# Kernel tuning notes

Measured on AMD Instinct MI355X. Metric: run time of the kernel, lower is better.

Reference implementation:

```python
import jax, jax.numpy as jnp
import numpy as np

NUM_EXPERTS = 64
TOP_K = 8
NORM_TOPK_PROB = True


def setup_inputs() -> dict:
    key = jax.random.key(0)
    k1, k2 = jax.random.split(key)
    hidden_states = jax.random.normal(k1, (8192, 4096), dtype=jnp.float32)
    gate_w = jax.random.normal(k2, (NUM_EXPERTS, 4096), dtype=jnp.float32) * (1.0 / np.sqrt(4096))
    return {"hidden_states": hidden_states, "gate_w": gate_w}


def reference(hidden_states, gate_w):
    # router_logits: (T, E) = hidden @ gate_w.T
    router_logits = jnp.einsum('th,eh->te', hidden_states, gate_w)
    # softmax in float32 (matches F.softmax(..., dtype=torch.float32))
    router_probs = jax.nn.softmax(router_logits.astype(jnp.float32), axis=-1)
    # top-k selection (descending, like torch.topk)
    expert_weights, expert_indices = jax.lax.top_k(router_probs, TOP_K)
    if NORM_TOPK_PROB:
        expert_weights = expert_weights / jnp.sum(expert_weights, axis=-1, keepdims=True)
    expert_weights = expert_weights.astype(hidden_states.dtype)
    # load-balancing loss: N_e * sum_i f_i * p_i
    num_tokens = router_probs.shape[0]
    one_hot = jax.nn.one_hot(expert_indices, NUM_EXPERTS, dtype=jnp.float32)  # (T, K, E)
    tokens_per_expert = one_hot.sum(axis=(0, 1))                              # (E,)
    f = tokens_per_expert / (num_tokens * TOP_K)
    p = router_probs.mean(axis=0)
    aux_loss = NUM_EXPERTS * jnp.sum(f * p)
    return (expert_weights, expert_indices, aux_loss)
```

## Files before the change

### kernel.cpp

```cpp
#include <hip/hip_runtime.h>
#include <math.h>

#define HDIM 4096
#define NEXP 64
#define NTOK 8192
#define KSPLIT 8
#define KSLICE (HDIM / KSPLIT)
#define BM 128
#define CHUNK 32
#define NCHUNK (KSLICE / CHUNK)
#define ASTRIDE 40
#define SLICEOFF 1024
#define TPW 2

typedef short short8 __attribute__((ext_vector_type(8)));
typedef float f32x4 __attribute__((ext_vector_type(4)));

__device__ __forceinline__ void split2x3(float x0, float x1, int& h, int& md, int& lo) {
  unsigned u0 = __float_as_uint(x0), u1 = __float_as_uint(x1);
  unsigned h0 = u0 & 0xFFFF0000u, h1 = u1 & 0xFFFF0000u;
  float r0 = x0 - __uint_as_float(h0);
  float r1 = x1 - __uint_as_float(h1);
  unsigned m0 = __float_as_uint(r0) & 0xFFFF0000u;
  unsigned m1 = __float_as_uint(r1) & 0xFFFF0000u;
  float s0 = r0 - __uint_as_float(m0);
  float s1 = r1 - __uint_as_float(m1);
  h  = (int)((h0 >> 16) | h1);
  md = (int)((m0 >> 16) | m1);
  lo = (int)((__float_as_uint(s0) >> 16) | (__float_as_uint(s1) & 0xFFFF0000u));
}

__global__ __launch_bounds__(256, 3) void gemm_k(const float* __restrict__ A,
                                                 const float* __restrict__ W,
                                                 float* __restrict__ Lp,
                                                 int atomic_mode) {
  __shared__ __align__(16) short Ah[BM * ASTRIDE], Amid[BM * ASTRIDE], Alo[BM * ASTRIDE];
  __shared__ __align__(16) short Bh[NEXP * ASTRIDE], Bmid[NEXP * ASTRIDE], Blo[NEXP * ASTRIDE];
  const int tid = threadIdx.x;
  const int m_base = blockIdx.x * BM;
  const int k_base = blockIdx.y * KSLICE;
  float* Lout = Lp + (atomic_mode ? (size_t)0 : (size_t)blockIdx.y * NTOK * NEXP);

  const int srow = tid >> 2;
  const int skg = tid & 3;
  const float* gA0 = A + (size_t)(m_base + srow) * HDIM + k_base + skg * 8;
  const float* gA1 = gA0 + (size_t)64 * HDIM;
  const float* gB = W + (size_t)srow * HDIM + k_base + skg * 8;

  const int lane = tid & 63;
  const int wave = tid >> 6;
  const int l15 = lane & 15;
  const int quad = lane >> 4;
  const int wm = wave * 32;

  f32x4 acc[2][4];
#pragma unroll
  for (int mt = 0; mt < 2; ++mt)
#pragma unroll
    for (int nt = 0; nt < 4; ++nt) acc[mt][nt] = (f32x4){0.f, 0.f, 0.f, 0.f};

  float4 pa0[2], pa1[2], pb[2];
  auto gload = [&](int i) {
    const float* p = gA0 + i * CHUNK;
    pa0[0] = *(const float4*)(p);
    pa0[1] = *(const float4*)(p + 4);
    p = gA1 + i * CHUNK;
    pa1[0] = *(const float4*)(p);
    pa1[1] = *(const float4*)(p + 4);
    p = gB + i * CHUNK;
    pb[0] = *(const float4*)(p);
    pb[1] = *(const float4*)(p + 4);
  };
  auto convert_store = [&]() {
    const float fa0[8] = {pa0[0].x, pa0[0].y, pa0[0].z, pa0[0].w,
                          pa0[1].x, pa0[1].y, pa0[1].z, pa0[1].w};
    const float fa1[8] = {pa1[0].x, pa1[0].y, pa1[0].z, pa1[0].w,
                          pa1[1].x, pa1[1].y, pa1[1].z, pa1[1].w};
    const float fb[8] = {pb[0].x, pb[0].y, pb[0].z, pb[0].w,
                         pb[1].x, pb[1].y, pb[1].z, pb[1].w};
    int h[4], md[4], lo[4];
    int off = srow * ASTRIDE + skg * 8;
#pragma unroll
    for (int j = 0; j < 4; ++j) split2x3(fa0[2 * j], fa0[2 * j + 1], h[j], md[j], lo[j]);
    *(int4*)&Ah[off] = make_int4(h[0], h[1], h[2], h[3]);
    *(int4*)&Amid[off] = make_int4(md[0], md[1], md[2], md[3]);
    *(int4*)&Alo[off] = make_int4(lo[0], lo[1], lo[2], lo[3]);
#pragma unroll
    for (int j = 0; j < 4; ++j) split2x3(fa1[2 * j], fa1[2 * j + 1], h[j], md[j], lo[j]);
    int off1 = (srow + 64) * ASTRIDE + skg * 8;
    *(int4*)&Ah[off1] = make_int4(h[0], h[1], h[2], h[3]);
    *(int4*)&Amid[off1] = make_int4(md[0], md[1], md[2], md[3]);
    *(int4*)&Alo[off1] = make_int4(lo[0], lo[1], lo[2], lo[3]);
#pragma unroll
    for (int j = 0; j < 4; ++j) split2x3(fb[2 * j], fb[2 * j + 1], h[j], md[j], lo[j]);
    *(int4*)&Bh[off] = make_int4(h[0], h[1], h[2], h[3]);
    *(int4*)&Bmid[off] = make_int4(md[0], md[1], md[2], md[3]);
    *(int4*)&Blo[off] = make_int4(lo[0], lo[1], lo[2], lo[3]);
  };

  gload(0);
  convert_store();
  __syncthreads();

  for (int i = 0; i < NCHUNK; ++i) {
    if (i + 1 < NCHUNK) gload(i + 1);
    short8 fa[2][3];
#pragma unroll
    for (int mt = 0; mt < 2; ++mt) {
      const int r = (wm + mt * 16 + l15) * ASTRIDE + quad * 8;
      fa[mt][0] = *(const short8*)&Ah[r];
      fa[mt][1] = *(const short8*)&Amid[r];
      fa[mt][2] = *(const short8*)&Alo[r];
    }
#pragma unroll
    for (int nt = 0; nt < 4; ++nt) {
      const int r = (nt * 16 + l15) * ASTRIDE + quad * 8;
      const short8 bh = *(const short8*)&Bh[r];
      const short8 bm = *(const short8*)&Bmid[r];
      const short8 bl = *(const short8*)&Blo[r];
#pragma unroll
      for (int mt = 0; mt < 2; ++mt) {
        f32x4 c = acc[mt][nt];
        c = __builtin_amdgcn_mfma_f32_16x16x32_bf16(fa[mt][0], bh, c, 0, 0, 0);
        c = __builtin_amdgcn_mfma_f32_16x16x32_bf16(fa[mt][0], bm, c, 0, 0, 0);
        c = __builtin_amdgcn_mfma_f32_16x16x32_bf16(fa[mt][1], bh, c, 0, 0, 0);
        c = __builtin_amdgcn_mfma_f32_16x16x32_bf16(fa[mt][0], bl, c, 0, 0, 0);
        c = __builtin_amdgcn_mfma_f32_16x16x32_bf16(fa[mt][2], bh, c, 0, 0, 0);
        c = __builtin_amdgcn_mfma_f32_16x16x32_bf16(fa[mt][1], bm, c, 0, 0, 0);
        acc[mt][nt] = c;
      }
    }
    __syncthreads();
    if (i + 1 < NCHUNK) convert_store();
    __syncthreads();
  }

#pragma unroll
  for (int mt = 0; mt < 2; ++mt)
#pragma unroll
    for (int nt = 0; nt < 4; ++nt)
#pragma unroll
      for (int r = 0; r < 4; ++r) {
        const int m = m_base + wm + mt * 16 + quad * 4 + r;
        const int n = nt * 16 + l15;
        if (atomic_mode) atomicAdd(&Lout[(size_t)m * NEXP + n], acc[mt][nt][r]);
        else Lout[(size_t)m * NEXP + n] = acc[mt][nt][r];
      }
}

__global__ __launch_bounds__(256) void topk_k(const float* __restrict__ Lp, int nsl,
                                              float* __restrict__ out,
                                              float* __restrict__ auxbuf) {
  __shared__ float sl[4][64];
  __shared__ float s_aux[128];
  const int tid = threadIdx.x;
  const int wave = tid >> 6, lane = tid & 63;
  if (tid < 128) s_aux[tid] = 0.f;
  __syncthreads();

  for (int it = 0; it < TPW; ++it) {
    const int t = (blockIdx.x * 4 + wave) * TPW + it;
    float x = 0.f;
    for (int s = 0; s < nsl; ++s)
      x += Lp[(size_t)s * (NTOK * NEXP) + (size_t)t * NEXP + lane];
    sl[wave][lane] = x;

    float mx = x;
#pragma unroll
    for (int off = 32; off >= 1; off >>= 1)
      mx = fmaxf(mx, __shfl_xor(mx, off, 64));
    const float e = __expf(x - mx);
    float ssum = e;
#pragma unroll
    for (int off = 32; off >= 1; off >>= 1) ssum += __shfl_xor(ssum, off, 64);
    const float prob = e / ssum;

    __syncthreads();

    int cnt = 0;
#pragma unroll
    for (int c = 0; c < 4; ++c) {
      const float4 v0 = *(const float4*)&sl[wave][c * 16 + 0];
      const float4 v1 = *(const float4*)&sl[wave][c * 16 + 4];
      const float4 v2 = *(const float4*)&sl[wave][c * 16 + 8];
      const float4 v3 = *(const float4*)&sl[wave][c * 16 + 12];
      const float xv[16] = {v0.x, v0.y, v0.z, v0.w, v1.x, v1.y, v1.z, v1.w,
                            v2.x, v2.y, v2.z, v2.w, v3.x, v3.y, v3.z, v3.w};
#pragma unroll
      for (int j = 0; j < 16; ++j) {
        const int jj = c * 16 + j;
        cnt += (xv[j] > x) || (xv[j] == x && jj < lane);
      }
    }

    float tp = (cnt < 8) ? prob : 0.f;
    float tsum = tp;
#pragma unroll
    for (int off = 32; off >= 1; off >>= 1) tsum += __shfl_xor(tsum, off, 64);

    const int dst = cnt << 2;
    const float pv = __uint_as_float(
        (unsigned)__builtin_amdgcn_ds_permute(dst, (int)__float_as_uint(prob)));
    const int pi = __builtin_amdgcn_ds_permute(dst, lane);
    if (lane < 8) {
      out[(size_t)t * 8 + lane] = pv / tsum;
      out[(size_t)NTOK * 8 + (size_t)t * 8 + lane] = (float)pi;
    }
    atomicAdd(&s_aux[lane], prob);
    if (cnt < 8) atomicAdd(&s_aux[64 + lane], 1.f);
  }
  __syncthreads();
  if (tid < 128) atomicAdd(&auxbuf[(blockIdx.x & 7) * 128 + tid], s_aux[tid]);
}

__global__ void aux_k(const float* __restrict__ auxbuf, float* __restrict__ out) {
  const int e = threadIdx.x;
  float p = 0.f, f = 0.f;
#pragma unroll
  for (int c = 0; c < 8; ++c) {
    p += auxbuf[c * 128 + e];
    f += auxbuf[c * 128 + 64 + e];
  }
  p *= (1.f / (float)NTOK);
  f *= (1.f / ((float)NTOK * 8.f));
  float v = f * p;
#pragma unroll
  for (int off = 32; off >= 1; off >>= 1) v += __shfl_xor(v, off, 64);
  if (e == 0) out[2 * NTOK * 8] = 64.f * v;
}

extern "C" void kernel_launch(void* const* d_in, const int* in_sizes, int n_in,
                              void* d_out, int out_size, void* d_ws, size_t ws_size,
                              hipStream_t stream) {
  const float* hidden = (const float*)d_in[0];
  const float* gate = (const float*)d_in[1];
  float* out = (float*)d_out;
  float* ws = (float*)d_ws;
  float* auxbuf = ws;
  float* slices = ws + SLICEOFF;

  const size_t need = (size_t)SLICEOFF * 4 + (size_t)KSPLIT * NTOK * NEXP * 4;
  const int atomic_mode = (ws_size < need) ? 1 : 0;
  const int nsl = atomic_mode ? 1 : KSPLIT;

  if (atomic_mode)
    hipMemsetAsync(d_ws, 0, (size_t)SLICEOFF * 4 + (size_t)NTOK * NEXP * 4, stream);
  else
    hipMemsetAsync(d_ws, 0, (size_t)SLICEOFF * 4, stream);

  gemm_k<<<dim3(64, KSPLIT), 256, 0, stream>>>(hidden, gate, slices, atomic_mode);
  topk_k<<<NTOK / (4 * TPW), 256, 0, stream>>>(slices, nsl, out, auxbuf);
  aux_k<<<1, 64, 0, stream>>>(auxbuf, out);
}
```

Before: 217.6 us.

## Pre-split gate weights into bf16x3 layout and split A on the fly

Adds a small pre-kernel that splits gate_w into high, mid and low bf16 parts laid out per 32-wide K chunk. The GEMM then reads B fragments straight from global memory. A is staged in LDS as raw fp32 in a double buffer and split into bf16 parts per wave just before the MFMAs, which drops one barrier per iteration. The top-k slice reduction is also unrolled for the 8-slice case. This removes the per-block redundant conversion of B and some LDS traffic, at the cost of an extra launch, global B loads in the inner loop, and repeated A splitting across waves.

```diff
diff --git a/kernel.cpp b/kernel.cpp
--- a/kernel.cpp
+++ b/kernel.cpp
@@ -9,8 +9,12 @@
 #define BM 128
 #define CHUNK 32
 #define NCHUNK (KSLICE / CHUNK)
-#define ASTRIDE 40
-#define SLICEOFF 1024
+#define AROW 36
+#define PSTRIDE 2048
+#define CSTRIDE 6144
+#define AUXF 1024
+#define BSF 393216
+#define SLICEOFF (AUXF + BSF)
 #define TPW 2
 
 typedef short short8 __attribute__((ext_vector_type(8)));
@@ -30,22 +34,45 @@
   lo = (int)((__float_as_uint(s0) >> 16) | (__float_as_uint(s1) & 0xFFFF0000u));
 }
 
+__device__ __forceinline__ short8 pack_s8(int a, int b, int c, int d) {
+  union { int i[4]; short8 s; } u;
+  u.i[0] = a; u.i[1] = b; u.i[2] = c; u.i[3] = d;
+  return u.s;
+}
+
+__global__ void bsplit_k(const float* __restrict__ W, short* __restrict__ Bs) {
+  const int e = blockIdx.x;
+  const int tid = threadIdx.x;
+#pragma unroll
+  for (int it = 0; it < 2; ++it) {
+    const int k0 = tid * 16 + it * 8;
+    const float4 v0 = *(const float4*)&W[(size_t)e * HDIM + k0];
+    const float4 v1 = *(const float4*)&W[(size_t)e * HDIM + k0 + 4];
+    const float f[8] = {v0.x, v0.y, v0.z, v0.w, v1.x, v1.y, v1.z, v1.w};
+    int h[4], md[4], lo[4];
+#pragma unroll
+    for (int j = 0; j < 4; ++j) split2x3(f[2 * j], f[2 * j + 1], h[j], md[j], lo[j]);
+    const int c = k0 >> 5, kk = k0 & 31;
+    short* p = Bs + (size_t)c * CSTRIDE + (size_t)e * 32 + kk;
+    *(int4*)(p)               = make_int4(h[0], h[1], h[2], h[3]);
+    *(int4*)(p + PSTRIDE)     = make_int4(md[0], md[1], md[2], md[3]);
+    *(int4*)(p + 2 * PSTRIDE) = make_int4(lo[0], lo[1], lo[2], lo[3]);
+  }
+}
+
 __global__ __launch_bounds__(256, 3) void gemm_k(const float* __restrict__ A,
-                                                 const float* __restrict__ W,
+                                                 const short* __restrict__ Bs,
                                                  float* __restrict__ Lp,
                                                  int atomic_mode) {
-  __shared__ __align__(16) short Ah[BM * ASTRIDE], Amid[BM * ASTRIDE], Alo[BM * ASTRIDE];
-  __shared__ __align__(16) short Bh[NEXP * ASTRIDE], Bmid[NEXP * ASTRIDE], Blo[NEXP * ASTRIDE];
+  __shared__ __align__(16) float As[2][BM * AROW];
   const int tid = threadIdx.x;
   const int m_base = blockIdx.x * BM;
   const int k_base = blockIdx.y * KSLICE;
   float* Lout = Lp + (atomic_mode ? (size_t)0 : (size_t)blockIdx.y * NTOK * NEXP);
 
-  const int srow = tid >> 2;
-  const int skg = tid & 3;
-  const float* gA0 = A + (size_t)(m_base + srow) * HDIM + k_base + skg * 8;
-  const float* gA1 = gA0 + (size_t)64 * HDIM;
-  const float* gB = W + (size_t)srow * HDIM + k_base + skg * 8;
+  const int srow = tid >> 3;
+  const int sslot = tid & 7;
+  const float* gA = A + (size_t)(m_base + srow) * HDIM + k_base + sslot * 4;
 
   const int lane = tid & 63;
   const int wave = tid >> 6;
@@ -59,65 +86,49 @@
 #pragma unroll
     for (int nt = 0; nt < 4; ++nt) acc[mt][nt] = (f32x4){0.f, 0.f, 0.f, 0.f};
 
-  float4 pa0[2], pa1[2], pb[2];
+  float4 pre[4];
   auto gload = [&](int i) {
-    const float* p = gA0 + i * CHUNK;
-    pa0[0] = *(const float4*)(p);
-    pa0[1] = *(const float4*)(p + 4);
-    p = gA1 + i * CHUNK;
-    pa1[0] = *(const float4*)(p);
-    pa1[1] = *(const float4*)(p + 4);
-    p = gB + i * CHUNK;
-    pb[0] = *(const float4*)(p);
-    pb[1] = *(const float4*)(p + 4);
+#pragma unroll
+    for (int j = 0; j < 4; ++j)
+      pre[j] = *(const float4*)(gA + (size_t)(j * 32) * HDIM + i * CHUNK);
   };
-  auto convert_store = [&]() {
-    const float fa0[8] = {pa0[0].x, pa0[0].y, pa0[0].z, pa0[0].w,
-                          pa0[1].x, pa0[1].y, pa0[1].z, pa0[1].w};
-    const float fa1[8] = {pa1[0].x, pa1[0].y, pa1[0].z, pa1[0].w,
-                          pa1[1].x, pa1[1].y, pa1[1].z, pa1[1].w};
-    const float fb[8] = {pb[0].x, pb[0].y, pb[0].z, pb[0].w,
-                         pb[1].x, pb[1].y, pb[1].z, pb[1].w};
-    int h[4], md[4], lo[4];
-    int off = srow * ASTRIDE + skg * 8;
-#pragma unroll
-    for (int j = 0; j < 4; ++j) split2x3(fa0[2 * j], fa0[2 * j + 1], h[j], md[j], lo[j]);
-    *(int4*)&Ah[off] = make_int4(h[0], h[1], h[2], h[3]);
-    *(int4*)&Amid[off] = make_int4(md[0], md[1], md[2], md[3]);
-    *(int4*)&Alo[off] = make_int4(lo[0], lo[1], lo[2], lo[3]);
-#pragma unroll
-    for (int j = 0; j < 4; ++j) split2x3(fa1[2 * j], fa1[2 * j + 1], h[j], md[j], lo[j]);
-    int off1 = (srow + 64) * ASTRIDE + skg * 8;
-    *(int4*)&Ah[off1] = make_int4(h[0], h[1], h[2], h[3]);
-    *(int4*)&Amid[off1] = make_int4(md[0], md[1], md[2], md[3]);
-    *(int4*)&Alo[off1] = make_int4(lo[0], lo[1], lo[2], lo[3]);
-#pragma unroll
-    for (int j = 0; j < 4; ++j) split2x3(fb[2 * j], fb[2 * j + 1], h[j], md[j], lo[j]);
-    *(int4*)&Bh[off] = make_int4(h[0], h[1], h[2], h[3]);
-    *(int4*)&Bmid[off] = make_int4(md[0], md[1], md[2], md[3]);
-    *(int4*)&Blo[off] = make_int4(lo[0], lo[1], lo[2], lo[3]);
+  auto stage = [&](int buf) {
+#pragma unroll
+    for (int j = 0; j < 4; ++j)
+      *(float4*)&As[buf][(j * 32 + srow) * AROW + sslot * 4] = pre[j];
   };
 
   gload(0);
-  convert_store();
+  stage(0);
   __syncthreads();
+
+  const short* bbase = Bs + (size_t)(k_base >> 5) * CSTRIDE + (size_t)l15 * 32 + quad * 8;
 
   for (int i = 0; i < NCHUNK; ++i) {
     if (i + 1 < NCHUNK) gload(i + 1);
+    const int buf = i & 1;
+
     short8 fa[2][3];
 #pragma unroll
     for (int mt = 0; mt < 2; ++mt) {
-      const int r = (wm + mt * 16 + l15) * ASTRIDE + quad * 8;
-      fa[mt][0] = *(const short8*)&Ah[r];
-      fa[mt][1] = *(const short8*)&Amid[r];
-      fa[mt][2] = *(const short8*)&Alo[r];
-    }
+      const int r = (wm + mt * 16 + l15) * AROW + quad * 8;
+      const float4 a0 = *(const float4*)&As[buf][r];
+      const float4 a1 = *(const float4*)&As[buf][r + 4];
+      const float f[8] = {a0.x, a0.y, a0.z, a0.w, a1.x, a1.y, a1.z, a1.w};
+      int h[4], md[4], lo[4];
+#pragma unroll
+      for (int j = 0; j < 4; ++j) split2x3(f[2 * j], f[2 * j + 1], h[j], md[j], lo[j]);
+      fa[mt][0] = pack_s8(h[0], h[1], h[2], h[3]);
+      fa[mt][1] = pack_s8(md[0], md[1], md[2], md[3]);
+      fa[mt][2] = pack_s8(lo[0], lo[1], lo[2], lo[3]);
+    }
+
+    const short* bp = bbase + (size_t)i * CSTRIDE;
 #pragma unroll
     for (int nt = 0; nt < 4; ++nt) {
-      const int r = (nt * 16 + l15) * ASTRIDE + quad * 8;
-      const short8 bh = *(const short8*)&Bh[r];
-      const short8 bm = *(const short8*)&Bmid[r];
-      const short8 bl = *(const short8*)&Blo[r];
+      const short8 bh = *(const short8*)(bp + nt * (16 * 32));
+      const short8 bm = *(const short8*)(bp + nt * (16 * 32) + PSTRIDE);
+      const short8 bl = *(const short8*)(bp + nt * (16 * 32) + 2 * PSTRIDE);
 #pragma unroll
       for (int mt = 0; mt < 2; ++mt) {
         f32x4 c = acc[mt][nt];
@@ -130,8 +141,8 @@
         acc[mt][nt] = c;
       }
     }
-    __syncthreads();
-    if (i + 1 < NCHUNK) convert_store();
+
+    if (i + 1 < NCHUNK) stage(buf ^ 1);
     __syncthreads();
   }
 
@@ -161,8 +172,14 @@
   for (int it = 0; it < TPW; ++it) {
     const int t = (blockIdx.x * 4 + wave) * TPW + it;
     float x = 0.f;
-    for (int s = 0; s < nsl; ++s)
-      x += Lp[(size_t)s * (NTOK * NEXP) + (size_t)t * NEXP + lane];
+    if (nsl == 8) {
+#pragma unroll
+      for (int s = 0; s < 8; ++s)
+        x += Lp[(size_t)s * (NTOK * NEXP) + (size_t)t * NEXP + lane];
+    } else {
+      for (int s = 0; s < nsl; ++s)
+        x += Lp[(size_t)s * (NTOK * NEXP) + (size_t)t * NEXP + lane];
+    }
     sl[wave][lane] = x;
 
     float mx = x;
@@ -237,6 +254,7 @@
   float* out = (float*)d_out;
   float* ws = (float*)d_ws;
   float* auxbuf = ws;
+  short* Bs = (short*)(ws + AUXF);
   float* slices = ws + SLICEOFF;
 
   const size_t need = (size_t)SLICEOFF * 4 + (size_t)KSPLIT * NTOK * NEXP * 4;
@@ -246,9 +264,10 @@
   if (atomic_mode)
     hipMemsetAsync(d_ws, 0, (size_t)SLICEOFF * 4 + (size_t)NTOK * NEXP * 4, stream);
   else
-    hipMemsetAsync(d_ws, 0, (size_t)SLICEOFF * 4, stream);
-
-  gemm_k<<<dim3(64, KSPLIT), 256, 0, stream>>>(hidden, gate, slices, atomic_mode);
+    hipMemsetAsync(d_ws, 0, (size_t)AUXF * 4, stream);
+
+  bsplit_k<<<NEXP, 256, 0, stream>>>(gate, Bs);
+  gemm_k<<<dim3(64, KSPLIT), 256, 0, stream>>>(hidden, Bs, slices, atomic_mode);
   topk_k<<<NTOK / (4 * TPW), 256, 0, stream>>>(slices, nsl, out, auxbuf);
   aux_k<<<1, 64, 0, stream>>>(auxbuf, out);
 }
```

Result: slower. 282.3 us (+29.8%).
